# Kernel optimization log

Measured on AMD Instinct MI355X. Metric: run time of the kernel, lower is better.

Reference implementation:

```python
import jax, jax.numpy as jnp
import numpy as np

N_NODES = 100000
N_EDGES = 3200000
IN_DIM = 256
OUT_DIM = 128


def setup_inputs() -> dict:
    key = jax.random.key(0)
    k1, k2, k3, k4, k5 = jax.random.split(key, 5)
    # node features
    x = jax.random.normal(k1, (N_NODES, IN_DIM), dtype=jnp.float32)
    # glorot-uniform weight as in glorot_init
    init_range = np.sqrt(6.0 / (IN_DIM + OUT_DIM)).astype(np.float32)
    weight = jax.random.uniform(k2, (IN_DIM, OUT_DIM), dtype=jnp.float32,
                                minval=-init_range, maxval=init_range)
    # sparse adjacency in COO form: adj[dst, src] = edge_weight
    edge_src = jax.random.randint(k3, (N_EDGES,), 0, N_NODES, dtype=jnp.int64)
    edge_dst = jax.random.randint(k4, (N_EDGES,), 0, N_NODES, dtype=jnp.int64)
    edge_weight = jax.random.uniform(k5, (N_EDGES,), dtype=jnp.float32)
    return {"x": x, "weight": weight, "edge_weight": edge_weight,
            "edge_src": edge_src, "edge_dst": edge_dst}


def reference(x, weight, edge_weight, edge_src, edge_dst):
    # dense feature transform: [N, in] @ [in, out] -> [N, out]
    xw = x @ weight
    # sparse adjacency matmul (adj @ xw) as gather + weighted scatter-add
    msgs = xw[edge_src] * edge_weight[:, None]           # [E, out]
    agg = jax.ops.segment_sum(msgs, edge_dst, num_segments=N_NODES)
    # fused activation
    return jax.nn.relu(agg)
```

## Files before the change

kernel.cpp:

```cpp
#include <hip/hip_runtime.h>

#define IN_DIM 256
#define OUT_DIM 128
#define BM 64
#define BKG 64

#define BSHIFT 7
#define BNODES 128
#define MAXB2 832
#define EPT1 10
#define CHUNK1 2560
#define CAPB 4736
#define HCAP 2560
#define RPT 19

typedef __attribute__((ext_vector_type(4))) float floatx4;
typedef __attribute__((ext_vector_type(8))) short shortx8;

static __device__ __forceinline__ unsigned short f2bf(float f) {
  unsigned u = __float_as_uint(f);
  u += 0x7FFFu + ((u >> 16) & 1u);
  return (unsigned short)(u >> 16);
}

__global__ __launch_bounds__(256) void prep_kernel(
    const float* __restrict__ w, unsigned short* __restrict__ wt,
    int* __restrict__ btail, int nb2) {
  const int idx = blockIdx.x * 256 + threadIdx.x;
  const int k = idx >> 7;
  const int n = idx & 127;
  wt[n * IN_DIM + k] = f2bf(w[idx]);
  if (blockIdx.x == 0)
    for (int b = threadIdx.x; b < nb2; b += 256) btail[b] = 0;
}

__global__ __launch_bounds__(256) void fused_pg_kernel(
    const float* __restrict__ x, const unsigned short* __restrict__ wt,
    unsigned short* __restrict__ xw, int n_nodes,
    const int* __restrict__ esrc, const int* __restrict__ edst,
    const float* __restrict__ ew, int* __restrict__ btail,
    uint2* __restrict__ csr2, int n_edges, int nb2, int pblocks) {
  __shared__ __align__(16) union {
    struct {
      unsigned short As[BM][BKG + 8];
      unsigned short Bs[OUT_DIM][BKG + 8];
    } g;
    struct {
      uint2 srec[CHUNK1];
      int hcnt[MAXB2];
      int aux[MAXB2];
      int sh[256];
    } p;
  } sm;

  const int bid = blockIdx.x;
  const int P = pblocks;
  const int G = (int)gridDim.x - pblocks;
  bool is_part;
  int vb;
  if (P <= G) {
    if (bid < 2 * P) { is_part = !(bid & 1); vb = bid >> 1; }
    else             { is_part = false;      vb = bid - P; }
  } else {
    if (bid < 2 * G) { is_part = (bid & 1);  vb = bid >> 1; }
    else             { is_part = true;       vb = bid - G; }
  }

  const int t = threadIdx.x;

  if (is_part) {
    const int base = vb * CHUNK1;
    const int cn = min(CHUNK1, n_edges - base);

    for (int b = t; b < MAXB2; b += 256) sm.p.hcnt[b] = 0;
    __syncthreads();

    int dst[EPT1];
    unsigned xpk[EPT1];
#pragma unroll
    for (int i = 0; i < EPT1; ++i) {
      const int idx = t + i * 256;
      if (idx < cn) {
        const int e = base + idx;
        dst[i] = edst[e];
        unsigned wb = __float_as_uint(ew[e]);
        wb += 0x7FFFu + ((wb >> 16) & 1u);
        xpk[i] = ((wb >> 16) << 17) | (unsigned)esrc[e];
        atomicAdd(&sm.p.hcnt[((unsigned)dst[i]) >> BSHIFT], 1);
      } else {
        dst[i] = -1;
      }
    }
    __syncthreads();
    {
      const int b4 = 4 * t;
      int a0 = 0, a1 = 0, a2 = 0, a3 = 0;
      if (b4 < MAXB2) {
        a0 = sm.p.hcnt[b4];     a1 = sm.p.hcnt[b4 + 1];
        a2 = sm.p.hcnt[b4 + 2]; a3 = sm.p.hcnt[b4 + 3];
      }
      const int s = a0 + a1 + a2 + a3;
      sm.p.sh[t] = s;
      __syncthreads();
      for (int off = 1; off < 256; off <<= 1) {
        const int add = (t >= off) ? sm.p.sh[t - off] : 0;
        __syncthreads();
        sm.p.sh[t] += add;
        __syncthreads();
      }
      if (b4 < MAXB2) {
        int run = sm.p.sh[t] - s;
        sm.p.aux[b4] = run; run += a0;
        sm.p.aux[b4 + 1] = run; run += a1;
        sm.p.aux[b4 + 2] = run; run += a2;
        sm.p.aux[b4 + 3] = run;
      }
    }
    __syncthreads();
    for (int b = t; b < nb2; b += 256) {
      const int c = sm.p.hcnt[b];
      const int lo = sm.p.aux[b];
      int g = 0;
      if (c) g = b * CAPB + atomicAdd(&btail[b], c);
      sm.p.hcnt[b] = lo;
      sm.p.aux[b] = g - lo;
    }
    __syncthreads();
#pragma unroll
    for (int i = 0; i < EPT1; ++i)
      if (dst[i] >= 0) {
        const int bk = ((unsigned)dst[i]) >> BSHIFT;
        const int p = atomicAdd(&sm.p.hcnt[bk], 1);
        sm.p.srec[p] = make_uint2(xpk[i], (unsigned)dst[i]);
      }
    __syncthreads();
    for (int i = t; i < cn; i += 256) {
      const uint2 r = sm.p.srec[i];
      const int bk = r.y >> BSHIFT;
      const size_t pos = (size_t)(sm.p.aux[bk] + i);
      if (pos < (size_t)(bk + 1) * CAPB) csr2[pos] = r;
    }
  } else {
    const int wv = t >> 6;
    const int lane = t & 63;
    const int quad = lane >> 4;
    const int l16 = lane & 15;
    const int row0 = vb * BM;
    if (row0 >= n_nodes) return;

    floatx4 acc[4][2];
#pragma unroll
    for (int a = 0; a < 4; ++a)
#pragma unroll
      for (int b = 0; b < 2; ++b) acc[a][b] = (floatx4){0.f, 0.f, 0.f, 0.f};

    for (int k0 = 0; k0 < IN_DIM; k0 += BKG) {
      __syncthreads();
#pragma unroll
      for (int i = 0; i < 4; ++i) {
        const int idx = i * 256 + t;
        const int r = idx >> 4;
        const int kq = (idx & 15) * 4;
        int row = row0 + r;
        if (row >= n_nodes) row = n_nodes - 1;
        const float4 v = *(const float4*)(x + (size_t)row * IN_DIM + k0 + kq);
        ushort4 sv;
        sv.x = f2bf(v.x); sv.y = f2bf(v.y); sv.z = f2bf(v.z); sv.w = f2bf(v.w);
        *(ushort4*)&sm.g.As[r][kq] = sv;
      }
#pragma unroll
      for (int i = 0; i < 4; ++i) {
        const int idx16 = i * 256 + t;
        const int n = idx16 >> 3;
        const int off = (idx16 & 7) * 8;
        *(int4*)&sm.g.Bs[n][off] =
            *(const int4*)(wt + (size_t)n * IN_DIM + k0 + off);
      }
      __syncthreads();

#pragma unroll
      for (int kk = 0; kk < BKG; kk += 32) {
        shortx8 af[4];
#pragma unroll
        for (int tm = 0; tm < 4; ++tm)
          af[tm] = *(const shortx8*)&sm.g.As[tm * 16 + l16][kk + quad * 8];
        shortx8 bfr[2];
#pragma unroll
        for (int tn = 0; tn < 2; ++tn)
          bfr[tn] =
              *(const shortx8*)&sm.g.Bs[wv * 32 + tn * 16 + l16][kk + quad * 8];
#pragma unroll
        for (int tm = 0; tm < 4; ++tm)
#pragma unroll
          for (int tn = 0; tn < 2; ++tn)
            acc[tm][tn] = __builtin_amdgcn_mfma_f32_16x16x32_bf16(
                af[tm], bfr[tn], acc[tm][tn], 0, 0, 0);
      }
    }

#pragma unroll
    for (int tm = 0; tm < 4; ++tm)
#pragma unroll
      for (int tn = 0; tn < 2; ++tn)
#pragma unroll
        for (int r = 0; r < 4; ++r) {
          const int grow = row0 + tm * 16 + quad * 4 + r;
          const int gcol = wv * 32 + tn * 16 + l16;
          if (grow < n_nodes)
            xw[(size_t)grow * OUT_DIM + gcol] = f2bf(acc[tm][tn][r]);
        }
  }
}

struct AggSmem {
  unsigned xs[HCAP];
  int cnt[64];
  int cur[64];
  int sst[64];
  int sen[64];
  int sh[64];
};

__global__ __launch_bounds__(256) void sort_agg_kernel(
    const uint2* __restrict__ csr2, const int* __restrict__ btail,
    const unsigned short* __restrict__ xw, float* __restrict__ out,
    int n_nodes) {
  __shared__ __align__(16) AggSmem sm;
  const int t = threadIdx.x;

  const int nwg = (int)gridDim.x;
  const int q = nwg >> 3, r = nwg & 7;
  const int xcd = blockIdx.x & 7, bix = blockIdx.x >> 3;
  const int lb = (xcd < r ? xcd * (q + 1) : r * (q + 1) + (xcd - r) * q) + bix;

  const int bucket = lb >> 1;
  const int half = lb & 1;
  const int node0 = (bucket << BSHIFT) + half * 64;
  const size_t S = (size_t)bucket * CAPB;
  const int cnt = min(btail[bucket], CAPB);

  uint2 rec[RPT];
#pragma unroll
  for (int k = 0; k < RPT; ++k) {
    const int i = t + k * 256;
    rec[k] = (i < cnt) ? csr2[S + i] : make_uint2(0u, 0xFFFFFFFFu);
  }

  if (t < 64) sm.cnt[t] = 0;
  __syncthreads();
#pragma unroll
  for (int k = 0; k < RPT; ++k) {
    const unsigned y = rec[k].y;
    if (y != 0xFFFFFFFFu) {
      const unsigned yl = y & (BNODES - 1);
      if ((int)(yl >> 6) == half) atomicAdd(&sm.cnt[yl & 63], 1);
    }
  }
  __syncthreads();
  {
    const int s = (t < 64) ? sm.cnt[t] : 0;
    if (t < 64) sm.sh[t] = s;
    __syncthreads();
    for (int off = 1; off < 64; off <<= 1) {
      const int add = (t >= off && t < 64) ? sm.sh[t - off] : 0;
      __syncthreads();
      if (t < 64) sm.sh[t] += add;
      __syncthreads();
    }
    if (t < 64) {
      const int run = sm.sh[t] - s;
      sm.cur[t] = run;
      sm.sst[t] = run;
      sm.sen[t] = run + s;
    }
  }
  __syncthreads();
#pragma unroll
  for (int k = 0; k < RPT; ++k) {
    const uint2 rr = rec[k];
    if (rr.y != 0xFFFFFFFFu) {
      const unsigned yl = rr.y & (BNODES - 1);
      if ((int)(yl >> 6) == half) {
        const int p = atomicAdd(&sm.cur[yl & 63], 1);
        if (p < HCAP) sm.xs[p] = rr.x;
      }
    }
  }
  if (t < 64) sm.sh[t] = ((sm.sen[t] - sm.sst[t]) << 6) | t;
  __syncthreads();
  for (int kk = 2; kk <= 64; kk <<= 1) {
    for (int jj = kk >> 1; jj > 0; jj >>= 1) {
      if (t < 64) {
        const int ixj = t ^ jj;
        if (ixj > t) {
          const int a = sm.sh[t], b = sm.sh[ixj];
          const bool up = ((t & kk) == 0);
          if ((a > b) == up) { sm.sh[t] = b; sm.sh[ixj] = a; }
        }
      }
      __syncthreads();
    }
  }

  const int g = t >> 4;
  const int lane = t & 15;
  const int d8 = lane * 8;
  const unsigned short* __restrict__ xwd = xw + d8;

#pragma unroll
  for (int ii = 0; ii < 4; ++ii) {
    const int nl = sm.sh[g + (ii << 4)] & 63;
    const int node = node0 + nl;
    if (node >= n_nodes) continue;
    const int j0 = sm.sst[nl];
    const int j1 = min(sm.sen[nl], HCAP);

    float a0 = 0.f, a1 = 0.f, a2 = 0.f, a3 = 0.f;
    float a4 = 0.f, a5 = 0.f, a6 = 0.f, a7 = 0.f;

    int j = j0;
    for (; j + 8 <= j1; j += 8) {
      uint4 v[8];
      float wq[8];
#pragma unroll
      for (int u = 0; u < 8; ++u) {
        const unsigned p = sm.xs[j + u];
        v[u] = *(const uint4*)(xwd + (size_t)(p & 0x1FFFFu) * OUT_DIM);
        wq[u] = __uint_as_float((p >> 17) << 16);
      }
#pragma unroll
      for (int u = 0; u < 8; ++u) {
        a0 = fmaf(__uint_as_float(v[u].x << 16), wq[u], a0);
        a1 = fmaf(__uint_as_float(v[u].x & 0xFFFF0000u), wq[u], a1);
        a2 = fmaf(__uint_as_float(v[u].y << 16), wq[u], a2);
        a3 = fmaf(__uint_as_float(v[u].y & 0xFFFF0000u), wq[u], a3);
        a4 = fmaf(__uint_as_float(v[u].z << 16), wq[u], a4);
        a5 = fmaf(__uint_as_float(v[u].z & 0xFFFF0000u), wq[u], a5);
        a6 = fmaf(__uint_as_float(v[u].w << 16), wq[u], a6);
        a7 = fmaf(__uint_as_float(v[u].w & 0xFFFF0000u), wq[u], a7);
      }
    }
    for (; j < j1; ++j) {
      const unsigned p0 = sm.xs[j];
      const float w0 = __uint_as_float((p0 >> 17) << 16);
      const uint4 v0 = *(const uint4*)(xwd + (size_t)(p0 & 0x1FFFFu) * OUT_DIM);
      a0 = fmaf(__uint_as_float(v0.x << 16), w0, a0);
      a1 = fmaf(__uint_as_float(v0.x & 0xFFFF0000u), w0, a1);
      a2 = fmaf(__uint_as_float(v0.y << 16), w0, a2);
      a3 = fmaf(__uint_as_float(v0.y & 0xFFFF0000u), w0, a3);
      a4 = fmaf(__uint_as_float(v0.z << 16), w0, a4);
      a5 = fmaf(__uint_as_float(v0.z & 0xFFFF0000u), w0, a5);
      a6 = fmaf(__uint_as_float(v0.w << 16), w0, a6);
      a7 = fmaf(__uint_as_float(v0.w & 0xFFFF0000u), w0, a7);
    }

    float4 o0, o1;
    o0.x = fmaxf(a0, 0.f); o0.y = fmaxf(a1, 0.f);
    o0.z = fmaxf(a2, 0.f); o0.w = fmaxf(a3, 0.f);
    o1.x = fmaxf(a4, 0.f); o1.y = fmaxf(a5, 0.f);
    o1.z = fmaxf(a6, 0.f); o1.w = fmaxf(a7, 0.f);
    float* orow = out + (size_t)node * OUT_DIM + d8;
    *(float4*)orow = o0;
    *(float4*)(orow + 4) = o1;
  }
}

extern "C" void kernel_launch(void* const* d_in, const int* in_sizes, int n_in,
                              void* d_out, int out_size, void* d_ws,
                              size_t ws_size, hipStream_t stream) {
  const float* x    = (const float*)d_in[0];
  const float* w    = (const float*)d_in[1];
  const float* ew   = (const float*)d_in[2];
  const int*   esrc = (const int*)d_in[3];
  const int*   edst = (const int*)d_in[4];
  float* out = (float*)d_out;

  const int n_edges = in_sizes[2];
  const int n_nodes = out_size / OUT_DIM;
  const int nb2 = (n_nodes + BNODES - 1) >> BSHIFT;

  char* p = (char*)d_ws;
  unsigned short* xw = (unsigned short*)p;
  p += (size_t)n_nodes * OUT_DIM * sizeof(unsigned short);
  p = (char*)(((uintptr_t)p + 15) & ~(uintptr_t)15);
  unsigned short* wt = (unsigned short*)p;
  p += (size_t)OUT_DIM * IN_DIM * sizeof(unsigned short);
  p = (char*)(((uintptr_t)p + 15) & ~(uintptr_t)15);
  uint2* csr2 = (uint2*)p;  p += (size_t)nb2 * CAPB * sizeof(uint2);
  int* btail = (int*)p;     p += (size_t)nb2 * sizeof(int);

  prep_kernel<<<(IN_DIM * OUT_DIM) / 256, 256, 0, stream>>>(w, wt, btail, nb2);

  const int pblocks = (n_edges + CHUNK1 - 1) / CHUNK1;
  const int gblocks = (n_nodes + BM - 1) / BM;
  fused_pg_kernel<<<pblocks + gblocks, 256, 0, stream>>>(
      x, wt, xw, n_nodes, esrc, edst, ew, btail, csr2, n_edges, nb2, pblocks);

  sort_agg_kernel<<<2 * nb2, 256, 0, stream>>>(csr2, btail, xw, out, n_nodes);
}
```

Measured before the change: 350.7 us.

## Sub-sort edges by source-id range and software-pipeline gather loads

```diff
diff --git a/kernel.cpp b/kernel.cpp
--- a/kernel.cpp
+++ b/kernel.cpp
@@ -13,6 +13,7 @@
 #define CAPB 4736
 #define HCAP 2560
 #define RPT 19
+#define NPH 16
 
 typedef __attribute__((ext_vector_type(4))) float floatx4;
 typedef __attribute__((ext_vector_type(8))) short shortx8;
@@ -214,11 +215,12 @@
 
 struct AggSmem {
   unsigned xs[HCAP];
-  int cnt[64];
-  int cur[64];
+  int cur[64 * NPH];
+  int sh[256];
   int sst[64];
   int sen[64];
-  int sh[64];
+  int skey[64];
+  int tot;
 };
 
 __global__ __launch_bounds__(256) void sort_agg_kernel(
@@ -246,33 +248,44 @@
     rec[k] = (i < cnt) ? csr2[S + i] : make_uint2(0u, 0xFFFFFFFFu);
   }
 
-  if (t < 64) sm.cnt[t] = 0;
+  for (int i = t; i < 64 * NPH; i += 256) sm.cur[i] = 0;
   __syncthreads();
 #pragma unroll
   for (int k = 0; k < RPT; ++k) {
     const unsigned y = rec[k].y;
     if (y != 0xFFFFFFFFu) {
       const unsigned yl = y & (BNODES - 1);
-      if ((int)(yl >> 6) == half) atomicAdd(&sm.cnt[yl & 63], 1);
+      if ((int)(yl >> 6) == half) {
+        const int ph = (int)((rec[k].x & 0x1FFFFu) >> 13);
+        atomicAdd(&sm.cur[(int)(yl & 63) * NPH + ph], 1);
+      }
     }
   }
   __syncthreads();
   {
-    const int s = (t < 64) ? sm.cnt[t] : 0;
-    if (t < 64) sm.sh[t] = s;
-    __syncthreads();
-    for (int off = 1; off < 64; off <<= 1) {
-      const int add = (t >= off && t < 64) ? sm.sh[t - off] : 0;
-      __syncthreads();
-      if (t < 64) sm.sh[t] += add;
-      __syncthreads();
-    }
-    if (t < 64) {
-      const int run = sm.sh[t] - s;
-      sm.cur[t] = run;
-      sm.sst[t] = run;
-      sm.sen[t] = run + s;
-    }
+    const int b4 = 4 * t;
+    const int a0 = sm.cur[b4], a1 = sm.cur[b4 + 1];
+    const int a2 = sm.cur[b4 + 2], a3 = sm.cur[b4 + 3];
+    const int s = a0 + a1 + a2 + a3;
+    sm.sh[t] = s;
+    __syncthreads();
+    for (int off = 1; off < 256; off <<= 1) {
+      const int add = (t >= off) ? sm.sh[t - off] : 0;
+      __syncthreads();
+      sm.sh[t] += add;
+      __syncthreads();
+    }
+    int run = sm.sh[t] - s;
+    sm.cur[b4] = run; run += a0;
+    sm.cur[b4 + 1] = run; run += a1;
+    sm.cur[b4 + 2] = run; run += a2;
+    sm.cur[b4 + 3] = run;
+    if (t == 255) sm.tot = sm.sh[255];
+  }
+  __syncthreads();
+  if (t < 64) {
+    sm.sst[t] = sm.cur[t * NPH];
+    sm.sen[t] = (t == 63) ? sm.tot : sm.cur[(t + 1) * NPH];
   }
   __syncthreads();
 #pragma unroll
@@ -281,21 +294,22 @@
     if (rr.y != 0xFFFFFFFFu) {
       const unsigned yl = rr.y & (BNODES - 1);
       if ((int)(yl >> 6) == half) {
-        const int p = atomicAdd(&sm.cur[yl & 63], 1);
+        const int ph = (int)((rr.x & 0x1FFFFu) >> 13);
+        const int p = atomicAdd(&sm.cur[(int)(yl & 63) * NPH + ph], 1);
         if (p < HCAP) sm.xs[p] = rr.x;
       }
     }
   }
-  if (t < 64) sm.sh[t] = ((sm.sen[t] - sm.sst[t]) << 6) | t;
+  if (t < 64) sm.skey[t] = ((sm.sen[t] - sm.sst[t]) << 6) | t;
   __syncthreads();
   for (int kk = 2; kk <= 64; kk <<= 1) {
     for (int jj = kk >> 1; jj > 0; jj >>= 1) {
       if (t < 64) {
         const int ixj = t ^ jj;
         if (ixj > t) {
-          const int a = sm.sh[t], b = sm.sh[ixj];
+          const int a = sm.skey[t], b = sm.skey[ixj];
           const bool up = ((t & kk) == 0);
-          if ((a > b) == up) { sm.sh[t] = b; sm.sh[ixj] = a; }
+          if ((a > b) == up) { sm.skey[t] = b; sm.skey[ixj] = a; }
         }
       }
       __syncthreads();
@@ -309,7 +323,7 @@
 
 #pragma unroll
   for (int ii = 0; ii < 4; ++ii) {
-    const int nl = sm.sh[g + (ii << 4)] & 63;
+    const int nl = sm.skey[g + (ii << 4)] & 63;
     const int node = node0 + nl;
     if (node >= n_nodes) continue;
     const int j0 = sm.sst[nl];
@@ -319,14 +333,41 @@
     float a4 = 0.f, a5 = 0.f, a6 = 0.f, a7 = 0.f;
 
     int j = j0;
-    for (; j + 8 <= j1; j += 8) {
+    const int n8 = (j1 - j0) & ~7;
+    if (n8 > 0) {
       uint4 v[8];
       float wq[8];
 #pragma unroll
       for (int u = 0; u < 8; ++u) {
-        const unsigned p = sm.xs[j + u];
+        const unsigned p = sm.xs[j0 + u];
         v[u] = *(const uint4*)(xwd + (size_t)(p & 0x1FFFFu) * OUT_DIM);
         wq[u] = __uint_as_float((p >> 17) << 16);
+      }
+      for (j = j0 + 8; j < j0 + n8; j += 8) {
+        uint4 nv[8];
+        float nw[8];
+#pragma unroll
+        for (int u = 0; u < 8; ++u) {
+          const unsigned p = sm.xs[j + u];
+          nv[u] = *(const uint4*)(xwd + (size_t)(p & 0x1FFFFu) * OUT_DIM);
+          nw[u] = __uint_as_float((p >> 17) << 16);
+        }
+#pragma unroll
+        for (int u = 0; u < 8; ++u) {
+          a0 = fmaf(__uint_as_float(v[u].x << 16), wq[u], a0);
+          a1 = fmaf(__uint_as_float(v[u].x & 0xFFFF0000u), wq[u], a1);
+          a2 = fmaf(__uint_as_float(v[u].y << 16), wq[u], a2);
+          a3 = fmaf(__uint_as_float(v[u].y & 0xFFFF0000u), wq[u], a3);
+          a4 = fmaf(__uint_as_float(v[u].z << 16), wq[u], a4);
+          a5 = fmaf(__uint_as_float(v[u].z & 0xFFFF0000u), wq[u], a5);
+          a6 = fmaf(__uint_as_float(v[u].w << 16), wq[u], a6);
+          a7 = fmaf(__uint_as_float(v[u].w & 0xFFFF0000u), wq[u], a7);
+        }
+#pragma unroll
+        for (int u = 0; u < 8; ++u) {
+          v[u] = nv[u];
+          wq[u] = nw[u];
+        }
       }
 #pragma unroll
       for (int u = 0; u < 8; ++u) {
@@ -339,6 +380,7 @@
         a6 = fmaf(__uint_as_float(v[u].w << 16), wq[u], a6);
         a7 = fmaf(__uint_as_float(v[u].w & 0xFFFF0000u), wq[u], a7);
       }
+      j = j0 + n8;
     }
     for (; j < j1; ++j) {
       const unsigned p0 = sm.xs[j];
```

Result: no change. 345.8 us (-1.4%).

## Enlarge GEMM tile to 128 rows and software-pipeline gather loads in aggregation

Applied to the files above, without the earlier changes.

```diff
diff --git a/kernel.cpp b/kernel.cpp
--- a/kernel.cpp
+++ b/kernel.cpp
@@ -2,7 +2,7 @@
 
 #define IN_DIM 256
 #define OUT_DIM 128
-#define BM 64
+#define BMG 128
 #define BKG 64
 
 #define BSHIFT 7
@@ -42,7 +42,7 @@
     uint2* __restrict__ csr2, int n_edges, int nb2, int pblocks) {
   __shared__ __align__(16) union {
     struct {
-      unsigned short As[BM][BKG + 8];
+      unsigned short As[BMG][BKG + 8];
       unsigned short Bs[OUT_DIM][BKG + 8];
     } g;
     struct {
@@ -142,22 +142,24 @@
     }
   } else {
     const int wv = t >> 6;
+    const int wr = wv >> 1;
+    const int wc = wv & 1;
     const int lane = t & 63;
     const int quad = lane >> 4;
     const int l16 = lane & 15;
-    const int row0 = vb * BM;
+    const int row0 = vb * BMG;
     if (row0 >= n_nodes) return;
 
-    floatx4 acc[4][2];
+    floatx4 acc[4][4];
 #pragma unroll
     for (int a = 0; a < 4; ++a)
 #pragma unroll
-      for (int b = 0; b < 2; ++b) acc[a][b] = (floatx4){0.f, 0.f, 0.f, 0.f};
+      for (int b = 0; b < 4; ++b) acc[a][b] = (floatx4){0.f, 0.f, 0.f, 0.f};
 
     for (int k0 = 0; k0 < IN_DIM; k0 += BKG) {
       __syncthreads();
 #pragma unroll
-      for (int i = 0; i < 4; ++i) {
+      for (int i = 0; i < 8; ++i) {
         const int idx = i * 256 + t;
         const int r = idx >> 4;
         const int kq = (idx & 15) * 4;
@@ -183,16 +185,17 @@
         shortx8 af[4];
 #pragma unroll
         for (int tm = 0; tm < 4; ++tm)
-          af[tm] = *(const shortx8*)&sm.g.As[tm * 16 + l16][kk + quad * 8];
-        shortx8 bfr[2];
-#pragma unroll
-        for (int tn = 0; tn < 2; ++tn)
+          af[tm] =
+              *(const shortx8*)&sm.g.As[wr * 64 + tm * 16 + l16][kk + quad * 8];
+        shortx8 bfr[4];
+#pragma unroll
+        for (int tn = 0; tn < 4; ++tn)
           bfr[tn] =
-              *(const shortx8*)&sm.g.Bs[wv * 32 + tn * 16 + l16][kk + quad * 8];
+              *(const shortx8*)&sm.g.Bs[wc * 64 + tn * 16 + l16][kk + quad * 8];
 #pragma unroll
         for (int tm = 0; tm < 4; ++tm)
 #pragma unroll
-          for (int tn = 0; tn < 2; ++tn)
+          for (int tn = 0; tn < 4; ++tn)
             acc[tm][tn] = __builtin_amdgcn_mfma_f32_16x16x32_bf16(
                 af[tm], bfr[tn], acc[tm][tn], 0, 0, 0);
       }
@@ -201,11 +204,11 @@
 #pragma unroll
     for (int tm = 0; tm < 4; ++tm)
 #pragma unroll
-      for (int tn = 0; tn < 2; ++tn)
+      for (int tn = 0; tn < 4; ++tn)
 #pragma unroll
         for (int r = 0; r < 4; ++r) {
-          const int grow = row0 + tm * 16 + quad * 4 + r;
-          const int gcol = wv * 32 + tn * 16 + l16;
+          const int grow = row0 + wr * 64 + tm * 16 + quad * 4 + r;
+          const int gcol = wc * 64 + tn * 16 + l16;
           if (grow < n_nodes)
             xw[(size_t)grow * OUT_DIM + gcol] = f2bf(acc[tm][tn][r]);
         }
@@ -319,14 +322,41 @@
     float a4 = 0.f, a5 = 0.f, a6 = 0.f, a7 = 0.f;
 
     int j = j0;
-    for (; j + 8 <= j1; j += 8) {
+    const int n8 = (j1 - j0) & ~7;
+    if (n8 > 0) {
       uint4 v[8];
       float wq[8];
 #pragma unroll
       for (int u = 0; u < 8; ++u) {
-        const unsigned p = sm.xs[j + u];
+        const unsigned p = sm.xs[j0 + u];
         v[u] = *(const uint4*)(xwd + (size_t)(p & 0x1FFFFu) * OUT_DIM);
         wq[u] = __uint_as_float((p >> 17) << 16);
+      }
+      for (j = j0 + 8; j < j0 + n8; j += 8) {
+        uint4 nv[8];
+        float nw[8];
+#pragma unroll
+        for (int u = 0; u < 8; ++u) {
+          const unsigned p = sm.xs[j + u];
+          nv[u] = *(const uint4*)(xwd + (size_t)(p & 0x1FFFFu) * OUT_DIM);
+          nw[u] = __uint_as_float((p >> 17) << 16);
+        }
+#pragma unroll
+        for (int u = 0; u < 8; ++u) {
+          a0 = fmaf(__uint_as_float(v[u].x << 16), wq[u], a0);
+          a1 = fmaf(__uint_as_float(v[u].x & 0xFFFF0000u), wq[u], a1);
+          a2 = fmaf(__uint_as_float(v[u].y << 16), wq[u], a2);
+          a3 = fmaf(__uint_as_float(v[u].y & 0xFFFF0000u), wq[u], a3);
+          a4 = fmaf(__uint_as_float(v[u].z << 16), wq[u], a4);
+          a5 = fmaf(__uint_as_float(v[u].z & 0xFFFF0000u), wq[u], a5);
+          a6 = fmaf(__uint_as_float(v[u].w << 16), wq[u], a6);
+          a7 = fmaf(__uint_as_float(v[u].w & 0xFFFF0000u), wq[u], a7);
+        }
+#pragma unroll
+        for (int u = 0; u < 8; ++u) {
+          v[u] = nv[u];
+          wq[u] = nw[u];
+        }
       }
 #pragma unroll
       for (int u = 0; u < 8; ++u) {
@@ -339,6 +369,7 @@
         a6 = fmaf(__uint_as_float(v[u].w << 16), wq[u], a6);
         a7 = fmaf(__uint_as_float(v[u].w & 0xFFFF0000u), wq[u], a7);
       }
+      j = j0 + n8;
     }
     for (; j < j1; ++j) {
       const unsigned p0 = sm.xs[j];
@@ -392,7 +423,7 @@
   prep_kernel<<<(IN_DIM * OUT_DIM) / 256, 256, 0, stream>>>(w, wt, btail, nb2);
 
   const int pblocks = (n_edges + CHUNK1 - 1) / CHUNK1;
-  const int gblocks = (n_nodes + BM - 1) / BM;
+  const int gblocks = (n_nodes + BMG - 1) / BMG;
   fused_pg_kernel<<<pblocks + gblocks, 256, 0, stream>>>(
       x, wt, xw, n_nodes, esrc, edst, ew, btail, csr2, n_edges, nb2, pblocks);
 
```

After: 337.0 us. 1.04x faster.
